# Optimization experiments

Hardware: AMD Instinct MI355X
Metric: run time of the kernel (lower is better)

Reference implementation:

```python
import jax, jax.numpy as jnp
import numpy as np
import math

HEAD_NUM = 16


def _split_qkv(qkv, head_num):
    # torch: rearrange(qkv, 'b t (d k h) -> k b h t d', k=3, h=head_num)
    B, T, E3 = qkv.shape
    d = E3 // (3 * head_num)
    qkv = qkv.reshape(B, T, d, 3, head_num)        # (b,t,d,k,h)
    qkv = jnp.transpose(qkv, (3, 0, 4, 1, 2))       # (k,b,h,t,d)
    return qkv[0], qkv[1], qkv[2]


def setup_inputs() -> dict:
    key = jax.random.key(0)
    ks = jax.random.split(key, 6)
    B, T, E = 4, 1024, 1024
    return {
        "x": jax.random.normal(ks[0], (B, T, E), dtype=jnp.float32),
        "y": jax.random.normal(ks[1], (B, T, E), dtype=jnp.float32),
        "Wqkv1": jax.random.normal(ks[2], (3 * E, E), dtype=jnp.float32) * 0.02,
        "Wqkv2": jax.random.normal(ks[3], (3 * E, E), dtype=jnp.float32) * 0.02,
        "Wout1": jax.random.normal(ks[4], (E, E), dtype=jnp.float32) * 0.02,
        "Wout2": jax.random.normal(ks[5], (E, E), dtype=jnp.float32) * 0.02,
    }


def reference(x, y, Wqkv1, Wqkv2, Wout1, Wout2):
    B, T, E = x.shape
    H = HEAD_NUM
    dk = math.sqrt(E / H)

    qkv1 = x @ Wqkv1.T                              # (B,T,3E)
    qkv2 = y @ Wqkv2.T
    q1, k1, v1 = _split_qkv(qkv1, H)                # each (B,H,T,d)
    q2, k2, v2 = _split_qkv(qkv2, H)

    # cross attention: stream-2 queries attend to stream-1 keys/values and vice versa
    energy1 = jnp.einsum('bhid,bhjd->bhij', q2, k1) / dk
    energy2 = jnp.einsum('bhid,bhjd->bhij', q1, k2) / dk
    attn1 = jax.nn.softmax(energy1, axis=-1)
    attn2 = jax.nn.softmax(energy2, axis=-1)

    xo = jnp.einsum('bhij,bhjd->bhid', attn1, v1)   # (B,H,T,d)
    yo = jnp.einsum('bhij,bhjd->bhid', attn2, v2)
    xo = jnp.transpose(xo, (0, 2, 1, 3)).reshape(B, T, E)  # b t (h d)
    yo = jnp.transpose(yo, (0, 2, 1, 3)).reshape(B, T, E)

    return xo @ Wout1.T, yo @ Wout2.T
```

## Files before the change

kernel.cpp:

```cpp
#include <hip/hip_runtime.h>
#include <hip/hip_bf16.h>

typedef __hip_bfloat16 bf16;
typedef __attribute__((ext_vector_type(8))) short short8;
typedef __attribute__((ext_vector_type(4))) short short4v;
typedef __attribute__((ext_vector_type(4))) float f32x4;

#define MFMA_BF16(a, b, c) __builtin_amdgcn_mfma_f32_16x16x32_bf16((a), (b), (c), 0, 0, 0)

#define QSCALE 0.1803368860111270f

__device__ __forceinline__ short f2bf(float f) {
    union { bf16 h; short s; } u;
    u.h = __float2bfloat16(f);
    return u.s;
}

#if defined(__has_builtin) && __has_builtin(__builtin_amdgcn_cvt_pk_bf16_f32)
typedef __attribute__((ext_vector_type(2))) __bf16 bf16x2_t;
__device__ __forceinline__ unsigned int pk2(float a, float b) {
    union { bf16x2_t v; unsigned int u; } x;
    x.v = __builtin_amdgcn_cvt_pk_bf16_f32(a, b);
    return x.u;
}
#else
__device__ __forceinline__ unsigned int pk2(float a, float b) {
    union { bf16 h[2]; unsigned int u; } x;
    x.h[0] = __float2bfloat16(a);
    x.h[1] = __float2bfloat16(b);
    return x.u;
}
#endif

__global__ void cvt_fused(const float* __restrict__ x, const float* __restrict__ y,
                          const float* __restrict__ wo1, const float* __restrict__ wo2,
                          const float* __restrict__ wq1, const float* __restrict__ wq2,
                          bf16* __restrict__ ox, bf16* __restrict__ oy,
                          bf16* __restrict__ oo1, bf16* __restrict__ oo2,
                          bf16* __restrict__ oq1, bf16* __restrict__ oq2) {
    const int yb = blockIdx.y;
    if (yb < 4) {
        int i = blockIdx.x * 256 + threadIdx.x;
        const float* src; bf16* dst; int n4;
        switch (yb) {
            case 0:  src = x;   dst = ox;  n4 = 1048576; break;
            case 1:  src = y;   dst = oy;  n4 = 1048576; break;
            case 2:  src = wo1; dst = oo1; n4 = 262144;  break;
            default: src = wo2; dst = oo2; n4 = 262144;  break;
        }
        if (i >= n4) return;
        float4 f = reinterpret_cast<const float4*>(src)[i];
        short4v s;
        s.x = f2bf(f.x); s.y = f2bf(f.y); s.z = f2bf(f.z); s.w = f2bf(f.w);
        reinterpret_cast<short4v*>(dst)[i] = s;
    } else {
        const int np = blockIdx.x;
        if (np >= 3072) return;
        const int comp = np >> 10, rem = np & 1023, h = rem >> 6, d = rem & 63;
        const int srow = d * 48 + comp * 16 + h;
        const float* src = ((yb == 5) ? wq2 : wq1) + (long)srow * 1024;
        bf16* dst = ((yb == 5) ? oq2 : oq1) + (long)np * 1024;
        const float sc = (comp == 0) ? QSCALE : 1.0f;
        int t = threadIdx.x;
        float4 f = reinterpret_cast<const float4*>(src)[t];
        short4v s;
        s.x = f2bf(f.x * sc); s.y = f2bf(f.y * sc); s.z = f2bf(f.z * sc); s.w = f2bf(f.w * sc);
        reinterpret_cast<short4v*>(dst)[t] = s;
    }
}

template <int MODE>
__global__ __launch_bounds__(256)
void gemm_k(const bf16* __restrict__ A0g, const bf16* __restrict__ B0g,
            void* o0a, void* o0b, void* o0c,
            const bf16* __restrict__ A1g, const bf16* __restrict__ B1g,
            void* o1a, void* o1b, void* o1c, int N) {
    __shared__ short smem[20480];
    const int z = blockIdx.z;
    const short* A = reinterpret_cast<const short*>(z ? A1g : A0g);
    const short* B = reinterpret_cast<const short*>(z ? B1g : B0g);
    const int tid  = threadIdx.x;
    const int lane = tid & 63;
    const int w    = tid >> 6;
    const int wr   = w >> 1;
    const int wc   = w & 1;
    const int quad = lane >> 4;
    const int l16  = lane & 15;
    const long bM = (long)blockIdx.y * 128;

    f32x4 acc[4][4] = {};

    const int srow = tid >> 2;
    const int sch  = (tid & 3) * 8;
    const short* Ag0 = A + (bM + srow) * 1024 + sch;
    const short* Ag1 = Ag0 + 64 * 1024;
    const short* Bg0 = B + ((long)blockIdx.x * 128 + srow) * 1024 + sch;
    const short* Bg1 = Bg0 + 64 * 1024;
    const int sbase = srow * 40 + sch;

    {
        short8 a0 = *reinterpret_cast<const short8*>(Ag0);
        short8 a1 = *reinterpret_cast<const short8*>(Ag1);
        short8 b0 = *reinterpret_cast<const short8*>(Bg0);
        short8 b1 = *reinterpret_cast<const short8*>(Bg1);
        *reinterpret_cast<short8*>(&smem[sbase]) = a0;
        *reinterpret_cast<short8*>(&smem[sbase + 64 * 40]) = a1;
        *reinterpret_cast<short8*>(&smem[sbase + 5120]) = b0;
        *reinterpret_cast<short8*>(&smem[sbase + 5120 + 64 * 40]) = b1;
    }
    __syncthreads();

    for (int iter = 0; iter < 32; ++iter) {
        const int cur = iter & 1;
        short8 pa0, pa1, pb0, pb1;
        if (iter < 31) {
            const int off = (iter + 1) * 32;
            pa0 = *reinterpret_cast<const short8*>(Ag0 + off);
            pa1 = *reinterpret_cast<const short8*>(Ag1 + off);
            pb0 = *reinterpret_cast<const short8*>(Bg0 + off);
            pb1 = *reinterpret_cast<const short8*>(Bg1 + off);
        }
        const short* Ab = smem + cur * 10240;
        const short* Bb = Ab + 5120;

        short8 af[4], bfr[4];
#pragma unroll
        for (int mt = 0; mt < 4; ++mt)
            af[mt] = *reinterpret_cast<const short8*>(&Ab[(wr * 64 + mt * 16 + l16) * 40 + quad * 8]);
#pragma unroll
        for (int nt = 0; nt < 4; ++nt)
            bfr[nt] = *reinterpret_cast<const short8*>(&Bb[(wc * 64 + nt * 16 + l16) * 40 + quad * 8]);
#pragma unroll
        for (int mt = 0; mt < 4; ++mt)
#pragma unroll
            for (int nt = 0; nt < 4; ++nt)
                acc[mt][nt] = MFMA_BF16(af[mt], bfr[nt], acc[mt][nt]);

        if (iter < 31) {
            short* Sn = smem + (cur ^ 1) * 10240 + sbase;
            *reinterpret_cast<short8*>(Sn) = pa0;
            *reinterpret_cast<short8*>(Sn + 64 * 40) = pa1;
            *reinterpret_cast<short8*>(Sn + 5120) = pb0;
            *reinterpret_cast<short8*>(Sn + 5120 + 64 * 40) = pb1;
        }
        __syncthreads();
    }

    if (MODE == 1) {
        float* C = reinterpret_cast<float*>(z ? o1a : o0a);
        const long crow = bM + wr * 64 + quad * 4;
        const long ccol = (long)blockIdx.x * 128 + wc * 64 + l16;
#pragma unroll
        for (int mt = 0; mt < 4; ++mt)
#pragma unroll
            for (int nt = 0; nt < 4; ++nt)
#pragma unroll
                for (int r = 0; r < 4; ++r)
                    C[(crow + mt * 16 + r) * (long)N + ccol + nt * 16] = acc[mt][nt][r];
        return;
    }

    if (blockIdx.x < 16) {
        short* dst = reinterpret_cast<short*>(blockIdx.x >= 8 ? (z ? o1b : o0b)
                                                              : (z ? o1a : o0a));
        const int hd0 = (int)(blockIdx.x & 7) * 128 + wc * 64;
        const int b = (int)(bM >> 10);
        const int t0 = ((int)bM & 1023) + wr * 64 + quad * 4;
#pragma unroll
        for (int nt = 0; nt < 4; ++nt) {
            const int hd = hd0 + nt * 16 + l16;
            const int h = hd >> 6, d = hd & 63;
            short* dp = dst + ((long)(b * 16 + h) * 1024) * 64 + d;
#pragma unroll
            for (int mt = 0; mt < 4; ++mt)
#pragma unroll
                for (int r = 0; r < 4; ++r)
                    dp[(long)(t0 + mt * 16 + r) * 64] = f2bf(acc[mt][nt][r]);
        }
    } else {
        short* vT = reinterpret_cast<short*>(z ? o1c : o0c);
        const int h = ((int)blockIdx.x - 16) * 2 + wc;
        const int b = (int)(bM >> 10);
        const int tb = ((int)bM & 1023) + wr * 64;
        short* ws = smem + w * 4608;
#pragma unroll
        for (int nt = 0; nt < 4; ++nt)
#pragma unroll
            for (int mt = 0; mt < 4; ++mt) {
                uint2 uu;
                uu.x = pk2(acc[mt][nt][0], acc[mt][nt][1]);
                uu.y = pk2(acc[mt][nt][2], acc[mt][nt][3]);
                *reinterpret_cast<uint2*>(&ws[(nt * 16 + l16) * 72 + mt * 16 + quad * 4]) = uu;
            }
        short* vbase = vT + (long)(b * 16 + h) * 64 * 1024;
#pragma unroll
        for (int p = 0; p < 8; ++p) {
            const int d = p * 8 + (lane >> 3);
            const int ch = (lane & 7) * 8;
            short8 v = *reinterpret_cast<const short8*>(&ws[d * 72 + ch]);
            *reinterpret_cast<short8*>(&vbase[(long)d * 1024 + tb + ch]) = v;
        }
    }
}

__global__ __launch_bounds__(256)
void attn_kernel(const bf16* __restrict__ q0g, const bf16* __restrict__ k0g,
                 const bf16* __restrict__ v0g, bf16* __restrict__ o0g,
                 const bf16* __restrict__ q1g, const bf16* __restrict__ k1g,
                 const bf16* __restrict__ v1g, bf16* __restrict__ o1g) {
    __shared__ short smem[20480];
    const int bh = blockIdx.x;
    const int qt = blockIdx.y;
    const int z = blockIdx.z;
    const int b = bh >> 4, h = bh & 15;
    const int tid = threadIdx.x, lane = tid & 63, w = tid >> 6;
    const int quad = lane >> 4, l16 = lane & 15;

    const short* Qb = reinterpret_cast<const short*>(z ? q1g : q0g) + (long)bh * 1024 * 64;
    const short* Kb = reinterpret_cast<const short*>(z ? k1g : k0g) + (long)bh * 1024 * 64;
    const short* Vb = reinterpret_cast<const short*>(z ? v1g : v0g) + (long)bh * 64 * 1024;
    short* Ob = reinterpret_cast<short*>(z ? o1g : o0g);

    short8 qb[2][2];
#pragma unroll
    for (int qg = 0; qg < 2; ++qg) {
        const short* Qp = Qb + (long)(qt * 128 + qg * 64 + w * 16 + l16) * 64;
        qb[qg][0] = *reinterpret_cast<const short8*>(Qp + quad * 8);
        qb[qg][1] = *reinterpret_cast<const short8*>(Qp + 32 + quad * 8);
    }

    const int r0 = tid >> 3, c8 = (tid & 7) * 8;
    const short* Kp0 = Kb + (long)r0 * 64 + c8;
    const short* Kp1 = Kp0 + 32L * 64;
    const short* Vp0 = Vb + (long)r0 * 1024 + c8;
    const short* Vp1 = Vp0 + 32L * 1024;
    short* Ld = smem + r0 * 80 + c8;

    const int jbase = 8 * (l16 >> 2) + (l16 & 3);

    f32x4 o[2][4] = {};
    float li[2] = {0.f, 0.f};

    {
        short8 a = *reinterpret_cast<const short8*>(Kp0);
        short8 bq = *reinterpret_cast<const short8*>(Kp1);
        short8 c = *reinterpret_cast<const short8*>(Vp0);
        short8 d = *reinterpret_cast<const short8*>(Vp1);
        *reinterpret_cast<short8*>(Ld) = a;
        *reinterpret_cast<short8*>(Ld + 32 * 80) = bq;
        *reinterpret_cast<short8*>(Ld + 5120) = c;
        *reinterpret_cast<short8*>(Ld + 5120 + 32 * 80) = d;
    }
    __syncthreads();

    for (int iter = 0; iter < 16; ++iter) {
        const int cur = iter & 1;
        short8 pk0, pk1, pv0, pv1;
        if (iter < 15) {
            const long joff = (long)(iter + 1) * 64;
            pk0 = *reinterpret_cast<const short8*>(Kp0 + joff * 64);
            pk1 = *reinterpret_cast<const short8*>(Kp1 + joff * 64);
            pv0 = *reinterpret_cast<const short8*>(Vp0 + joff);
            pv1 = *reinterpret_cast<const short8*>(Vp1 + joff);
        }
        const short* Ks = smem + cur * 10240;
        const short* Vs = Ks + 5120;

        f32x4 st[2][4];
        const short* kbp = Ks + jbase * 80 + quad * 8;
#pragma unroll
        for (int g = 0; g < 4; ++g) {
            const int goff = (g >> 1) * 32 + (g & 1) * 4;
            short8 k0 = *reinterpret_cast<const short8*>(kbp + goff * 80);
            short8 k1 = *reinterpret_cast<const short8*>(kbp + goff * 80 + 32);
#pragma unroll
            for (int qg = 0; qg < 2; ++qg) {
                f32x4 zf = {0.f, 0.f, 0.f, 0.f};
                zf = MFMA_BF16(k0, qb[qg][0], zf);
                zf = MFMA_BF16(k1, qb[qg][1], zf);
                st[qg][g] = zf;
            }
        }

        union { unsigned int u[4]; short8 s; } f0[2], f1[2];
#pragma unroll
        for (int qg = 0; qg < 2; ++qg) {
            float p[4][4];
            float rs = 0.f;
#pragma unroll
            for (int g = 0; g < 4; ++g)
#pragma unroll
                for (int r = 0; r < 4; ++r) {
                    float e = exp2f(st[qg][g][r]);
                    p[g][r] = e;
                    rs += e;
                }
            li[qg] += rs;
            f0[qg].u[0] = pk2(p[0][0], p[0][1]); f0[qg].u[1] = pk2(p[0][2], p[0][3]);
            f0[qg].u[2] = pk2(p[1][0], p[1][1]); f0[qg].u[3] = pk2(p[1][2], p[1][3]);
            f1[qg].u[0] = pk2(p[2][0], p[2][1]); f1[qg].u[1] = pk2(p[2][2], p[2][3]);
            f1[qg].u[2] = pk2(p[3][0], p[3][1]); f1[qg].u[3] = pk2(p[3][2], p[3][3]);
        }

#pragma unroll
        for (int dt = 0; dt < 4; ++dt) {
            const short* vbp = Vs + (dt * 16 + l16) * 80 + quad * 8;
            short8 v0 = *reinterpret_cast<const short8*>(vbp);
            short8 v1 = *reinterpret_cast<const short8*>(vbp + 32);
#pragma unroll
            for (int qg = 0; qg < 2; ++qg) {
                o[qg][dt] = MFMA_BF16(v0, f0[qg].s, o[qg][dt]);
                o[qg][dt] = MFMA_BF16(v1, f1[qg].s, o[qg][dt]);
            }
        }

        if (iter < 15) {
            short* Ln = Ld + (cur ^ 1) * 10240;
            *reinterpret_cast<short8*>(Ln) = pk0;
            *reinterpret_cast<short8*>(Ln + 32 * 80) = pk1;
            *reinterpret_cast<short8*>(Ln + 5120) = pv0;
            *reinterpret_cast<short8*>(Ln + 5120 + 32 * 80) = pv1;
        }
        __syncthreads();
    }

#pragma unroll
    for (int qg = 0; qg < 2; ++qg) {
        li[qg] += __shfl_xor(li[qg], 16);
        li[qg] += __shfl_xor(li[qg], 32);
    }

#pragma unroll
    for (int qg = 0; qg < 2; ++qg) {
        short* Os = smem + qg * 5120 + w * 1280;
        const float rl = 1.0f / li[qg];
#pragma unroll
        for (int dt = 0; dt < 4; ++dt) {
            uint2 uu;
            uu.x = pk2(o[qg][dt][0] * rl, o[qg][dt][1] * rl);
            uu.y = pk2(o[qg][dt][2] * rl, o[qg][dt][3] * rl);
            *reinterpret_cast<uint2*>(&Os[l16 * 80 + dt * 16 + quad * 4]) = uu;
        }
#pragma unroll
        for (int p = 0; p < 2; ++p) {
            int row = p * 8 + (lane >> 3);
            int ch = (lane & 7) * 8;
            short8 v = *reinterpret_cast<const short8*>(&Os[row * 80 + ch]);
            *reinterpret_cast<short8*>(&Ob[((long)(b * 1024) + qt * 128 + qg * 64 + w * 16 + row) * 1024 + h * 64 + ch]) = v;
        }
    }
}

extern "C" void kernel_launch(void* const* d_in, const int* in_sizes, int n_in,
                              void* d_out, int out_size, void* d_ws, size_t ws_size,
                              hipStream_t stream) {
    const float* x     = (const float*)d_in[0];
    const float* y     = (const float*)d_in[1];
    const float* Wqkv1 = (const float*)d_in[2];
    const float* Wqkv2 = (const float*)d_in[3];
    const float* Wout1 = (const float*)d_in[4];
    const float* Wout2 = (const float*)d_in[5];

    char* ws = (char*)d_ws;
    bf16* Wqkv1b = (bf16*)(ws + 0);
    bf16* Wqkv2b = (bf16*)(ws + 6291456);
    bf16* Wout1b = (bf16*)(ws + 12582912);
    bf16* Wout2b = (bf16*)(ws + 14680064);
    bf16* xb     = (bf16*)(ws + 16777216);
    bf16* yb     = (bf16*)(ws + 25165824);
    bf16* q1     = (bf16*)(ws + 33554432);
    bf16* k1     = (bf16*)(ws + 41943040);
    bf16* v1T    = (bf16*)(ws + 50331648);
    bf16* q2     = (bf16*)(ws + 58720256);
    bf16* k2     = (bf16*)(ws + 67108864);
    bf16* v2T    = (bf16*)(ws + 75497472);
    bf16* xo     = xb;
    bf16* yo     = yb;

    cvt_fused<<<dim3(4096, 6), 256, 0, stream>>>(x, y, Wout1, Wout2, Wqkv1, Wqkv2,
                                                 xb, yb, Wout1b, Wout2b, Wqkv1b, Wqkv2b);

    gemm_k<0><<<dim3(24, 32, 2), 256, 0, stream>>>(xb, Wqkv1b, q1, k1, v1T,
                                                   yb, Wqkv2b, q2, k2, v2T, 3072);

    attn_kernel<<<dim3(64, 8, 2), 256, 0, stream>>>(q2, k1, v1T, xo,
                                                    q1, k2, v2T, yo);

    gemm_k<1><<<dim3(8, 32, 2), 256, 0, stream>>>(xo, Wout1b, (float*)d_out, nullptr, nullptr,
                                                  yo, Wout2b, ((float*)d_out) + 4194304, nullptr, nullptr,
                                                  1024);
}
```

Baseline: 270.3 us.

## Use direct global-to-LDS loads with XOR-swizzled layout in GEMM and attention

Replaces the register-staged global loads followed by LDS stores with the global_load_lds builtin, which writes 16-byte chunks straight into shared memory. Both kernels do this. The padded LDS rows (stride 40/80) become unpadded rows with an XOR swizzle on the chunk index to avoid bank conflicts, which also shrinks the shared-memory footprint. The aim is to cut register pressure and VALU/LDS-store instructions in the main loops. The risk is that correct ordering now depends on the compiler emitting the right vmcnt waits before the barrier, and the swizzle must match the per-lane writes exactly.

```diff
diff --git a/kernel.cpp b/kernel.cpp
--- a/kernel.cpp
+++ b/kernel.cpp
@@ -31,6 +31,12 @@
     return x.u;
 }
 #endif
+
+__device__ __forceinline__ void gload16(const void* g, void* l) {
+    __builtin_amdgcn_global_load_lds(
+        (const __attribute__((address_space(1))) unsigned int*)g,
+        (__attribute__((address_space(3))) unsigned int*)l, 16, 0, 0);
+}
 
 __global__ void cvt_fused(const float* __restrict__ x, const float* __restrict__ y,
                           const float* __restrict__ wo1, const float* __restrict__ wo2,
@@ -90,59 +96,50 @@
 
     f32x4 acc[4][4] = {};
 
-    const int srow = tid >> 2;
-    const int sch  = (tid & 3) * 8;
-    const short* Ag0 = A + (bM + srow) * 1024 + sch;
-    const short* Ag1 = Ag0 + 64 * 1024;
-    const short* Bg0 = B + ((long)blockIdx.x * 128 + srow) * 1024 + sch;
-    const short* Bg1 = Bg0 + 64 * 1024;
-    const int sbase = srow * 40 + sch;
+    const int sr  = lane >> 2;
+    const int scs = ((lane & 3) ^ (sr & 3)) * 8;
+    const short* Ag0 = A + (bM + 32 * w + sr) * 1024 + scs;
+    const short* Ag1 = Ag0 + 16 * 1024;
+    const short* Bg0 = B + ((long)blockIdx.x * 128 + 32 * w + sr) * 1024 + scs;
+    const short* Bg1 = Bg0 + 16 * 1024;
+
+    const int sq = (quad ^ (l16 & 3)) * 8;
 
     {
-        short8 a0 = *reinterpret_cast<const short8*>(Ag0);
-        short8 a1 = *reinterpret_cast<const short8*>(Ag1);
-        short8 b0 = *reinterpret_cast<const short8*>(Bg0);
-        short8 b1 = *reinterpret_cast<const short8*>(Bg1);
-        *reinterpret_cast<short8*>(&smem[sbase]) = a0;
-        *reinterpret_cast<short8*>(&smem[sbase + 64 * 40]) = a1;
-        *reinterpret_cast<short8*>(&smem[sbase + 5120]) = b0;
-        *reinterpret_cast<short8*>(&smem[sbase + 5120 + 64 * 40]) = b1;
+        short* sb = smem;
+        gload16(Ag0, sb + w * 1024);
+        gload16(Ag1, sb + w * 1024 + 512);
+        gload16(Bg0, sb + 4096 + w * 1024);
+        gload16(Bg1, sb + 4096 + w * 1024 + 512);
     }
     __syncthreads();
 
     for (int iter = 0; iter < 32; ++iter) {
         const int cur = iter & 1;
-        short8 pa0, pa1, pb0, pb1;
         if (iter < 31) {
-            const int off = (iter + 1) * 32;
-            pa0 = *reinterpret_cast<const short8*>(Ag0 + off);
-            pa1 = *reinterpret_cast<const short8*>(Ag1 + off);
-            pb0 = *reinterpret_cast<const short8*>(Bg0 + off);
-            pb1 = *reinterpret_cast<const short8*>(Bg1 + off);
-        }
-        const short* Ab = smem + cur * 10240;
-        const short* Bb = Ab + 5120;
+            const int koff = (iter + 1) * 32;
+            short* sb = smem + (cur ^ 1) * 8192;
+            gload16(Ag0 + koff, sb + w * 1024);
+            gload16(Ag1 + koff, sb + w * 1024 + 512);
+            gload16(Bg0 + koff, sb + 4096 + w * 1024);
+            gload16(Bg1 + koff, sb + 4096 + w * 1024 + 512);
+        }
+        const short* Ab = smem + cur * 8192;
+        const short* Bb = Ab + 4096;
 
         short8 af[4], bfr[4];
 #pragma unroll
         for (int mt = 0; mt < 4; ++mt)
-            af[mt] = *reinterpret_cast<const short8*>(&Ab[(wr * 64 + mt * 16 + l16) * 40 + quad * 8]);
+            af[mt] = *reinterpret_cast<const short8*>(&Ab[(wr * 64 + mt * 16 + l16) * 32 + sq]);
 #pragma unroll
         for (int nt = 0; nt < 4; ++nt)
-            bfr[nt] = *reinterpret_cast<const short8*>(&Bb[(wc * 64 + nt * 16 + l16) * 40 + quad * 8]);
+            bfr[nt] = *reinterpret_cast<const short8*>(&Bb[(wc * 64 + nt * 16 + l16) * 32 + sq]);
 #pragma unroll
         for (int mt = 0; mt < 4; ++mt)
 #pragma unroll
             for (int nt = 0; nt < 4; ++nt)
                 acc[mt][nt] = MFMA_BF16(af[mt], bfr[nt], acc[mt][nt]);
 
-        if (iter < 31) {
-            short* Sn = smem + (cur ^ 1) * 10240 + sbase;
-            *reinterpret_cast<short8*>(Sn) = pa0;
-            *reinterpret_cast<short8*>(Sn + 64 * 40) = pa1;
-            *reinterpret_cast<short8*>(Sn + 5120) = pb0;
-            *reinterpret_cast<short8*>(Sn + 5120 + 64 * 40) = pb1;
-        }
         __syncthreads();
     }
 
@@ -208,7 +205,7 @@
                  const bf16* __restrict__ v0g, bf16* __restrict__ o0g,
                  const bf16* __restrict__ q1g, const bf16* __restrict__ k1g,
                  const bf16* __restrict__ v1g, bf16* __restrict__ o1g) {
-    __shared__ short smem[20480];
+    __shared__ short smem[16384];
     const int bh = blockIdx.x;
     const int qt = blockIdx.y;
     const int z = blockIdx.z;
@@ -229,12 +226,12 @@
         qb[qg][1] = *reinterpret_cast<const short8*>(Qp + 32 + quad * 8);
     }
 
-    const int r0 = tid >> 3, c8 = (tid & 7) * 8;
-    const short* Kp0 = Kb + (long)r0 * 64 + c8;
-    const short* Kp1 = Kp0 + 32L * 64;
-    const short* Vp0 = Vb + (long)r0 * 1024 + c8;
-    const short* Vp1 = Vp0 + 32L * 1024;
-    short* Ld = smem + r0 * 80 + c8;
+    const int r8  = lane >> 3;
+    const int sc8 = ((lane & 7) ^ r8) * 8;
+    const short* Kg0 = Kb + (long)(16 * w + r8) * 64 + sc8;
+    const short* Kg1 = Kg0 + 8 * 64;
+    const short* Vg0 = Vb + (long)(16 * w + r8) * 1024 + sc8;
+    const short* Vg1 = Vg0 + 8 * 1024;
 
     const int jbase = 8 * (l16 >> 2) + (l16 & 3);
 
@@ -242,37 +239,37 @@
     float li[2] = {0.f, 0.f};
 
     {
-        short8 a = *reinterpret_cast<const short8*>(Kp0);
-        short8 bq = *reinterpret_cast<const short8*>(Kp1);
-        short8 c = *reinterpret_cast<const short8*>(Vp0);
-        short8 d = *reinterpret_cast<const short8*>(Vp1);
-        *reinterpret_cast<short8*>(Ld) = a;
-        *reinterpret_cast<short8*>(Ld + 32 * 80) = bq;
-        *reinterpret_cast<short8*>(Ld + 5120) = c;
-        *reinterpret_cast<short8*>(Ld + 5120 + 32 * 80) = d;
+        short* sb = smem;
+        gload16(Kg0, sb + w * 1024);
+        gload16(Kg1, sb + w * 1024 + 512);
+        gload16(Vg0, sb + 4096 + w * 1024);
+        gload16(Vg1, sb + 4096 + w * 1024 + 512);
     }
     __syncthreads();
 
     for (int iter = 0; iter < 16; ++iter) {
         const int cur = iter & 1;
-        short8 pk0, pk1, pv0, pv1;
         if (iter < 15) {
-            const long joff = (long)(iter + 1) * 64;
-            pk0 = *reinterpret_cast<const short8*>(Kp0 + joff * 64);
-            pk1 = *reinterpret_cast<const short8*>(Kp1 + joff * 64);
-            pv0 = *reinterpret_cast<const short8*>(Vp0 + joff);
-            pv1 = *reinterpret_cast<const short8*>(Vp1 + joff);
-        }
-        const short* Ks = smem + cur * 10240;
-        const short* Vs = Ks + 5120;
+            const long ko = (long)(iter + 1) * 4096;
+            const long vo = (long)(iter + 1) * 64;
+            short* sb = smem + (cur ^ 1) * 8192;
+            gload16(Kg0 + ko, sb + w * 1024);
+            gload16(Kg1 + ko, sb + w * 1024 + 512);
+            gload16(Vg0 + vo, sb + 4096 + w * 1024);
+            gload16(Vg1 + vo, sb + 4096 + w * 1024 + 512);
+        }
+        const short* Ks = smem + cur * 8192;
+        const short* Vs = Ks + 4096;
 
         f32x4 st[2][4];
-        const short* kbp = Ks + jbase * 80 + quad * 8;
 #pragma unroll
         for (int g = 0; g < 4; ++g) {
             const int goff = (g >> 1) * 32 + (g & 1) * 4;
-            short8 k0 = *reinterpret_cast<const short8*>(kbp + goff * 80);
-            short8 k1 = *reinterpret_cast<const short8*>(kbp + goff * 80 + 32);
+            const int row = jbase + goff;
+            const int s0 = (quad ^ (row & 7)) * 8;
+            const short* kr = Ks + row * 64;
+            short8 k0 = *reinterpret_cast<const short8*>(kr + s0);
+            short8 k1 = *reinterpret_cast<const short8*>(kr + (s0 ^ 32));
 #pragma unroll
             for (int qg = 0; qg < 2; ++qg) {
                 f32x4 zf = {0.f, 0.f, 0.f, 0.f};
@@ -304,9 +301,11 @@
 
 #pragma unroll
         for (int dt = 0; dt < 4; ++dt) {
-            const short* vbp = Vs + (dt * 16 + l16) * 80 + quad * 8;
-            short8 v0 = *reinterpret_cast<const short8*>(vbp);
-            short8 v1 = *reinterpret_cast<const short8*>(vbp + 32);
+            const int rv = dt * 16 + l16;
+            const int sv = (quad ^ (rv & 7)) * 8;
+            const short* vr = Vs + rv * 64;
+            short8 v0 = *reinterpret_cast<const short8*>(vr + sv);
+            short8 v1 = *reinterpret_cast<const short8*>(vr + (sv ^ 32));
 #pragma unroll
             for (int qg = 0; qg < 2; ++qg) {
                 o[qg][dt] = MFMA_BF16(v0, f0[qg].s, o[qg][dt]);
@@ -314,13 +313,6 @@
             }
         }
 
-        if (iter < 15) {
-            short* Ln = Ld + (cur ^ 1) * 10240;
-            *reinterpret_cast<short8*>(Ln) = pk0;
-            *reinterpret_cast<short8*>(Ln + 32 * 80) = pk1;
-            *reinterpret_cast<short8*>(Ln + 5120) = pv0;
-            *reinterpret_cast<short8*>(Ln + 5120 + 32 * 80) = pv1;
-        }
         __syncthreads();
     }
 
```

Measured after the change: 264.2 us. 2.2% less time.
